# Performance work log

Measured on AMD Instinct MI355X. Metric: run time of the kernel, lower is better.

The kernel has to match this reference:

```python
import jax, jax.numpy as jnp
import numpy as np

EPS = 1e-08

def setup_inputs() -> dict:
    key = jax.random.key(0)
    k1, = jax.random.split(key, 1)
    B, C, H, W = 8, 128, 128, 256
    inp = jax.random.normal(k1, (B, C, H, W), dtype=jnp.float32)
    gain = jnp.ones((1, C, 1, 1), dtype=jnp.float32)
    bias = jnp.zeros((1, C, 1, 1), dtype=jnp.float32)
    return {"inp": inp, "gain": gain, "bias": bias}

def reference(inp, gain, bias):
    # LayerNorm over the last dim (W), then per-channel affine.
    # (Original torch code computes mean/var via a Python loop of adds;
    #  the intended math is a plain last-dim mean/variance.)
    mean = jnp.mean(inp, axis=-1, keepdims=True)
    centered = inp - mean
    var = jnp.mean(centered * centered, axis=-1, keepdims=True)
    std = jnp.sqrt(var + EPS)
    x = centered / std
    return x * gain + bias
```

## Files before the change

kernel.cpp:

```cpp
#include <hip/hip_runtime.h>
#include <hip/hip_bf16.h>


#define W_DIM 256
#define H_DIM 128
#define C_DIM 128
#define EPS 1e-8f

__global__ __launch_bounds__(256) void tLNv2_kernel(
    const float* __restrict__ inp,
    const float* __restrict__ gain,
    const float* __restrict__ bias,
    float* __restrict__ out)
{
    const int lane = threadIdx.x & 63;
    const int wave = threadIdx.x >> 6;
    const long long row = (long long)blockIdx.x * 4 + wave;

    const float4* __restrict__ in4 = (const float4*)(inp + row * W_DIM);
    float4 v = in4[lane];

    float s  = v.x + v.y + v.z + v.w;
    float sq = v.x * v.x + v.y * v.y + v.z * v.z + v.w * v.w;

    #pragma unroll
    for (int off = 1; off < 64; off <<= 1) {
        s  += __shfl_xor(s,  off, 64);
        sq += __shfl_xor(sq, off, 64);
    }

    const float mean = s * (1.0f / (float)W_DIM);
    const float var  = sq * (1.0f / (float)W_DIM) - mean * mean;
    const float rstd = rsqrtf(var + EPS);

    const int c = (int)((row >> 7) & (C_DIM - 1));
    const float g = gain[c];
    const float b = bias[c];

    float4 o;
    o.x = (v.x - mean) * rstd * g + b;
    o.y = (v.y - mean) * rstd * g + b;
    o.z = (v.z - mean) * rstd * g + b;
    o.w = (v.w - mean) * rstd * g + b;

    ((float4*)(out + row * W_DIM))[lane] = o;
}

extern "C" void kernel_launch(void* const* d_in, const int* in_sizes, int n_in,
                              void* d_out, int out_size, void* d_ws, size_t ws_size,
                              hipStream_t stream)
{
    const float* inp  = (const float*)d_in[0];
    const float* gain = (const float*)d_in[1];
    const float* bias = (const float*)d_in[2];
    float* out = (float*)d_out;

    const long long rows = (long long)in_sizes[0] / W_DIM;
    const int blocks = (int)(rows / 4);

    tLNv2_kernel<<<blocks, 256, 0, stream>>>(inp, gain, bias, out);
}
```

Before: 223.0 us.

## Use persistent grid-stride waves with next-row prefetch in LayerNorm

Replaces the one-row-per-wave launch with a grid capped at 2048 blocks, in which each wave loops over rows with a stride. Each iteration issues the load for the next row before reducing and writing the current one. This is meant to hide global memory latency and cut block launch overhead. It lowers the number of waves in flight, so achieved bandwidth now depends on per-wave memory parallelism and on the grid cap.

Result: slower. 233.6 us (+4.8%).

```diff
diff --git a/kernel.cpp b/kernel.cpp
--- a/kernel.cpp
+++ b/kernel.cpp
@@ -1,49 +1,62 @@
 #include <hip/hip_runtime.h>
-#include <hip/hip_bf16.h>
 
 
 #define W_DIM 256
-#define H_DIM 128
 #define C_DIM 128
 #define EPS 1e-8f
 
-__global__ __launch_bounds__(256) void tLNv2_kernel(
+typedef float f32x4 __attribute__((ext_vector_type(4)));
+
+__global__ __launch_bounds__(256) void tLNv3_kernel(
     const float* __restrict__ inp,
     const float* __restrict__ gain,
     const float* __restrict__ bias,
-    float* __restrict__ out)
+    float* __restrict__ out,
+    const int rows, const int wave_stride)
 {
     const int lane = threadIdx.x & 63;
-    const int wave = threadIdx.x >> 6;
-    const long long row = (long long)blockIdx.x * 4 + wave;
+    int row = (int)(blockIdx.x << 2) + (threadIdx.x >> 6);
+    if (row >= rows) return;
 
-    const float4* __restrict__ in4 = (const float4*)(inp + row * W_DIM);
-    float4 v = in4[lane];
+    const f32x4* __restrict__ in4  = (const f32x4*)inp;
+    f32x4* __restrict__       out4 = (f32x4*)out;
 
-    float s  = v.x + v.y + v.z + v.w;
-    float sq = v.x * v.x + v.y * v.y + v.z * v.z + v.w * v.w;
+    f32x4 v = in4[(size_t)row * 64 + lane];
 
-    #pragma unroll
-    for (int off = 1; off < 64; off <<= 1) {
-        s  += __shfl_xor(s,  off, 64);
-        sq += __shfl_xor(sq, off, 64);
+    for (;;) {
+        const int  nrow      = row + wave_stride;
+        const bool have_next = (nrow < rows);
+        f32x4 vn = {};
+        if (have_next) vn = in4[(size_t)nrow * 64 + lane];
+
+        float s  = v.x + v.y + v.z + v.w;
+        float sq = v.x * v.x + v.y * v.y + v.z * v.z + v.w * v.w;
+
+        #pragma unroll
+        for (int off = 1; off < 64; off <<= 1) {
+            s  += __shfl_xor(s,  off, 64);
+            sq += __shfl_xor(sq, off, 64);
+        }
+
+        const float mean = s * (1.0f / (float)W_DIM);
+        const float var  = sq * (1.0f / (float)W_DIM) - mean * mean;
+        const float rstd = rsqrtf(var + EPS);
+
+        const int   c = (row >> 7) & (C_DIM - 1);
+        const float g = gain[c];
+        const float b = bias[c];
+
+        f32x4 o;
+        o.x = (v.x - mean) * rstd * g + b;
+        o.y = (v.y - mean) * rstd * g + b;
+        o.z = (v.z - mean) * rstd * g + b;
+        o.w = (v.w - mean) * rstd * g + b;
+        out4[(size_t)row * 64 + lane] = o;
+
+        if (!have_next) break;
+        v   = vn;
+        row = nrow;
     }
-
-    const float mean = s * (1.0f / (float)W_DIM);
-    const float var  = sq * (1.0f / (float)W_DIM) - mean * mean;
-    const float rstd = rsqrtf(var + EPS);
-
-    const int c = (int)((row >> 7) & (C_DIM - 1));
-    const float g = gain[c];
-    const float b = bias[c];
-
-    float4 o;
-    o.x = (v.x - mean) * rstd * g + b;
-    o.y = (v.y - mean) * rstd * g + b;
-    o.z = (v.z - mean) * rstd * g + b;
-    o.w = (v.w - mean) * rstd * g + b;
-
-    ((float4*)(out + row * W_DIM))[lane] = o;
 }
 
 extern "C" void kernel_launch(void* const* d_in, const int* in_sizes, int n_in,
@@ -55,8 +68,11 @@
     const float* bias = (const float*)d_in[2];
     float* out = (float*)d_out;
 
-    const long long rows = (long long)in_sizes[0] / W_DIM;
-    const int blocks = (int)(rows / 4);
+    const int rows = in_sizes[0] / W_DIM;
 
-    tLNv2_kernel<<<blocks, 256, 0, stream>>>(inp, gain, bias, out);
+    int blocks = (rows + 3) / 4;
+    if (blocks > 2048) blocks = 2048;
+    const int wave_stride = blocks * 4;
+
+    tLNv3_kernel<<<blocks, 256, 0, stream>>>(inp, gain, bias, out, rows, wave_stride);
 }
```

## Process one row per 16-lane quarter-wave with four float4 loads per thread

Applied to the files above, without the earlier changes.

Each wave now handles four rows, with 16 lanes per row and four strided float4 loads per thread. This cuts the shuffle reduction from six steps to four, gives each thread more loads in flight, and quarters the block count. The affine step is folded into a single fma per element using precomputed scale and offset. The cost is more registers per thread and fewer waves overall for this memory-bound kernel.

Result: slower. 228.2 us (+2.3%).

```diff
diff --git a/kernel.cpp b/kernel.cpp
--- a/kernel.cpp
+++ b/kernel.cpp
@@ -1,30 +1,51 @@
 #include <hip/hip_runtime.h>
-#include <hip/hip_bf16.h>
 
 
 #define W_DIM 256
-#define H_DIM 128
 #define C_DIM 128
 #define EPS 1e-8f
 
-__global__ __launch_bounds__(256) void tLNv2_kernel(
+typedef float f32x4 __attribute__((ext_vector_type(4)));
+
+__global__ __launch_bounds__(256) void tLNv4_kernel(
     const float* __restrict__ inp,
     const float* __restrict__ gain,
     const float* __restrict__ bias,
-    float* __restrict__ out)
+    float* __restrict__ out,
+    const int rows)
 {
     const int lane = threadIdx.x & 63;
-    const int wave = threadIdx.x >> 6;
-    const long long row = (long long)blockIdx.x * 4 + wave;
+    const int sub  = lane & 15;
+    const int quad = lane >> 4;
+    const int grp  = (int)(blockIdx.x << 2) + (threadIdx.x >> 6);
 
-    const float4* __restrict__ in4 = (const float4*)(inp + row * W_DIM);
-    float4 v = in4[lane];
+    const int row = (grp << 2) + quad;
+    if (row >= rows) return;
 
-    float s  = v.x + v.y + v.z + v.w;
-    float sq = v.x * v.x + v.y * v.y + v.z * v.z + v.w * v.w;
+    const f32x4* __restrict__ in4  = (const f32x4*)inp;
+    f32x4* __restrict__       out4 = (f32x4*)out;
+
+    const size_t base = (size_t)row * 64 + sub;
+    f32x4 v0 = in4[base];
+    f32x4 v1 = in4[base + 16];
+    f32x4 v2 = in4[base + 32];
+    f32x4 v3 = in4[base + 48];
+
+    float s = (v0.x + v0.y) + (v0.z + v0.w)
+            + (v1.x + v1.y) + (v1.z + v1.w)
+            + (v2.x + v2.y) + (v2.z + v2.w)
+            + (v3.x + v3.y) + (v3.z + v3.w);
+    float sq = v0.x * v0.x;
+    sq = fmaf(v0.y, v0.y, sq); sq = fmaf(v0.z, v0.z, sq); sq = fmaf(v0.w, v0.w, sq);
+    sq = fmaf(v1.x, v1.x, sq); sq = fmaf(v1.y, v1.y, sq);
+    sq = fmaf(v1.z, v1.z, sq); sq = fmaf(v1.w, v1.w, sq);
+    sq = fmaf(v2.x, v2.x, sq); sq = fmaf(v2.y, v2.y, sq);
+    sq = fmaf(v2.z, v2.z, sq); sq = fmaf(v2.w, v2.w, sq);
+    sq = fmaf(v3.x, v3.x, sq); sq = fmaf(v3.y, v3.y, sq);
+    sq = fmaf(v3.z, v3.z, sq); sq = fmaf(v3.w, v3.w, sq);
 
     #pragma unroll
-    for (int off = 1; off < 64; off <<= 1) {
+    for (int off = 1; off < 16; off <<= 1) {
         s  += __shfl_xor(s,  off, 64);
         sq += __shfl_xor(sq, off, 64);
     }
@@ -33,17 +54,27 @@
     const float var  = sq * (1.0f / (float)W_DIM) - mean * mean;
     const float rstd = rsqrtf(var + EPS);
 
-    const int c = (int)((row >> 7) & (C_DIM - 1));
+    const int   c = (grp >> 5) & (C_DIM - 1);
     const float g = gain[c];
     const float b = bias[c];
 
-    float4 o;
-    o.x = (v.x - mean) * rstd * g + b;
-    o.y = (v.y - mean) * rstd * g + b;
-    o.z = (v.z - mean) * rstd * g + b;
-    o.w = (v.w - mean) * rstd * g + b;
+    const float a  = rstd * g;
+    const float bb = b - mean * a;
 
-    ((float4*)(out + row * W_DIM))[lane] = o;
+    f32x4 o0, o1, o2, o3;
+    o0.x = fmaf(v0.x, a, bb); o0.y = fmaf(v0.y, a, bb);
+    o0.z = fmaf(v0.z, a, bb); o0.w = fmaf(v0.w, a, bb);
+    o1.x = fmaf(v1.x, a, bb); o1.y = fmaf(v1.y, a, bb);
+    o1.z = fmaf(v1.z, a, bb); o1.w = fmaf(v1.w, a, bb);
+    o2.x = fmaf(v2.x, a, bb); o2.y = fmaf(v2.y, a, bb);
+    o2.z = fmaf(v2.z, a, bb); o2.w = fmaf(v2.w, a, bb);
+    o3.x = fmaf(v3.x, a, bb); o3.y = fmaf(v3.y, a, bb);
+    o3.z = fmaf(v3.z, a, bb); o3.w = fmaf(v3.w, a, bb);
+
+    out4[base]      = o0;
+    out4[base + 16] = o1;
+    out4[base + 32] = o2;
+    out4[base + 48] = o3;
 }
 
 extern "C" void kernel_launch(void* const* d_in, const int* in_sizes, int n_in,
@@ -55,8 +86,9 @@
     const float* bias = (const float*)d_in[2];
     float* out = (float*)d_out;
 
-    const long long rows = (long long)in_sizes[0] / W_DIM;
-    const int blocks = (int)(rows / 4);
+    const int rows   = in_sizes[0] / W_DIM;
+    const int groups = (rows + 3) / 4;
+    const int blocks = (groups + 3) / 4;
 
-    tLNv2_kernel<<<blocks, 256, 0, stream>>>(inp, gain, bias, out);
+    tLNv4_kernel<<<blocks, 256, 0, stream>>>(inp, gain, bias, out, rows);
 }
```
